# Optimization experiments

Measured on AMD Instinct MI355X. Metric: run time of the kernel, lower is better.

## Reference

```python
import jax, jax.numpy as jnp
import numpy as np

B, C_IN, C_OUT, N, K = 4, 64, 128, 81920, 10


def setup_inputs() -> dict:
    key = jax.random.key(0)
    k1, k2, k3, k4 = jax.random.split(key, 4)
    x = jax.random.normal(k1, (B, C_IN, N), dtype=jnp.float32)
    indices = jax.random.randint(k2, (N, K), 0, N, dtype=jnp.int64)
    # Conv2d(in, out, kernel=(1,K)) weight [C_out, C_in, 1, K] -> store as [C_out, C_in, K]
    fan_in = C_IN * K
    bound = 1.0 / np.sqrt(fan_in)
    W = jax.random.uniform(k3, (C_OUT, C_IN, K), jnp.float32, -bound, bound)
    b = jax.random.uniform(k4, (C_OUT,), jnp.float32, -bound, bound)
    return {"input": x, "indices": indices, "W": W, "b": b}


def reference(input, indices, W, b):
    # gather neighbor pixels: [B, C_in, N, K]
    col = input[:, :, indices]
    # 1xK conv == contraction over (C_in, K): [B, C_out, N]
    out = jnp.einsum('bcnk,ock->bon', col, W) + b[None, :, None]
    return out
```

## Files before the change

### kernel.cpp

```cpp
#include <hip/hip_runtime.h>
#include <hip/hip_bf16.h>
#include <stdint.h>

#define NPTS 81920
#define CIN  64
#define COUT 128
#define BATCH 4
#define KNB  10
#define CK   640
#define NT   64

typedef __attribute__((ext_vector_type(8))) short bf16x8;
typedef __attribute__((ext_vector_type(4))) float f32x4;

static __device__ __forceinline__ unsigned short f2bf(float f) {
    unsigned int u = __float_as_uint(f);
    u += 0x7fffu + ((u >> 16) & 1u);
    return (unsigned short)(u >> 16);
}

static __device__ __forceinline__ void gload16(const void* g, void* l) {
    __builtin_amdgcn_global_load_lds(
        (const __attribute__((address_space(1))) unsigned int*)g,
        (__attribute__((address_space(3))) unsigned int*)l, 16, 0, 0);
}

__global__ __launch_bounds__(256) void k_transpose(const float* __restrict__ x,
                                                   unsigned short* __restrict__ xT) {
    const int m = blockIdx.x * 256 + threadIdx.x;
    const int b = blockIdx.y;
    const float* xb = x + (size_t)b * CIN * NPTS + m;

    unsigned int v[CIN / 2];
    #pragma unroll
    for (int i = 0; i < CIN / 2; ++i) {
        float f0 = xb[(size_t)(2 * i) * NPTS];
        float f1 = xb[(size_t)(2 * i + 1) * NPTS];
        v[i] = (unsigned int)f2bf(f0) | ((unsigned int)f2bf(f1) << 16);
    }
    uint4* dst = (uint4*)(xT + ((size_t)m * BATCH + b) * CIN);
    #pragma unroll
    for (int i = 0; i < 8; ++i) {
        uint4 w; w.x = v[4*i]; w.y = v[4*i+1]; w.z = v[4*i+2]; w.w = v[4*i+3];
        dst[i] = w;
    }
}

__global__ __launch_bounds__(256) void k_wconv(const float* __restrict__ W,
                                               unsigned short* __restrict__ Wb) {
    const int e = blockIdx.x * 256 + threadIdx.x;
    const int j = e & 7;
    const int l = (e >> 3) & 63;
    const int f = (e >> 9) & 7;
    const int s = e >> 12;
    const int o = 16 * f + (l & 15);
    const int ck = s * 32 + 8 * (l >> 4) + j;
    const int k = ck >> 6;
    const int c = ck & 63;
    Wb[e] = f2bf(W[(o * CIN + c) * KNB + k]);
}

__global__ __launch_bounds__(512, 4) void k_main(const unsigned short* __restrict__ xT,
                                                 const unsigned short* __restrict__ Wb,
                                                 const float* __restrict__ bias,
                                                 const int* __restrict__ idx,
                                                 float* __restrict__ out) {
    __shared__ char smem[2][NT][256];

    const int t    = threadIdx.x;
    const int lane = t & 63;
    const int wv   = t >> 6;
    const int ln   = lane & 15;
    const int lg   = lane >> 4;
    const int bz   = blockIdx.y;
    const int nb   = blockIdx.x * NT;

    const char* xbase = (const char*)xT + bz * 256;
    const bf16x8* wbase = (const bf16x8*)Wb;

    f32x4 acc[4][2];
    #pragma unroll
    for (int j = 0; j < 4; ++j) {
        acc[j][0] = (f32x4){0.f, 0.f, 0.f, 0.f};
        acc[j][1] = (f32x4){0.f, 0.f, 0.f, 0.f};
    }

    #define STAGE(k)                                                            \
        {                                                                       \
            _Pragma("unroll")                                                   \
            for (int i = 0; i < 2; ++i) {                                       \
                const int row   = (wv << 3) + (i << 2) + (lane >> 4);           \
                const int nglob = nb + row;                                     \
                const int r     = idx[nglob * KNB + (k)];                       \
                const char* src = xbase + (size_t)r * 512 +                     \
                                  (((lane & 15) * 16) ^ ((row & 7) << 4));      \
                gload16(src, &smem[(k) & 1][(wv << 3) + (i << 2)][0]);          \
            }                                                                   \
        }

    STAGE(0);
    bf16x8 a0 = wbase[(0 * 8 + wv) * 64 + lane];
    bf16x8 a1 = wbase[(1 * 8 + wv) * 64 + lane];
    __syncthreads();

    #pragma unroll
    for (int k = 0; k < KNB; ++k) {
        if (k + 1 < KNB) STAGE(k + 1);
        bf16x8 a0n = a0, a1n = a1;
        if (k + 1 < KNB) {
            a0n = wbase[((2 * k + 2) * 8 + wv) * 64 + lane];
            a1n = wbase[((2 * k + 3) * 8 + wv) * 64 + lane];
        }
        #pragma unroll
        for (int h = 0; h < 2; ++h) {
            const bf16x8 a = h ? a1 : a0;
            #pragma unroll
            for (int j = 0; j < 4; ++j) {
                const int row = j * 16 + ln;
                const int sw  = (row & 7) << 4;
                #pragma unroll
                for (int bb = 0; bb < 2; ++bb) {
                    const int byte = bb * 128 + ((h * 64 + lg * 16) ^ sw);
                    const bf16x8 bf = *(const bf16x8*)&smem[k & 1][row][byte];
                    acc[j][bb] = __builtin_amdgcn_mfma_f32_16x16x32_bf16(
                        a, bf, acc[j][bb], 0, 0, 0);
                }
            }
        }
        __syncthreads();
        a0 = a0n; a1 = a1n;
    }
    #undef STAGE

    #pragma unroll
    for (int j = 0; j < 4; ++j) {
        const int n = nb + j * 16 + ln;
        #pragma unroll
        for (int bb = 0; bb < 2; ++bb) {
            const int b = bz * 2 + bb;
            #pragma unroll
            for (int r = 0; r < 4; ++r) {
                const int o = 16 * wv + 4 * lg + r;
                out[(size_t)(b * COUT + o) * NPTS + n] = acc[j][bb][r] + bias[o];
            }
        }
    }
}

extern "C" void kernel_launch(void* const* d_in, const int* in_sizes, int n_in,
                              void* d_out, int out_size, void* d_ws, size_t ws_size,
                              hipStream_t stream) {
    const float* x    = (const float*)d_in[0];
    const int*   idx  = (const int*)d_in[1];
    const float* W    = (const float*)d_in[2];
    const float* bias = (const float*)d_in[3];
    float* out = (float*)d_out;

    unsigned short* xT = (unsigned short*)d_ws;
    unsigned short* Wb = (unsigned short*)((char*)d_ws + (size_t)BATCH * NPTS * CIN * 2);

    k_transpose<<<dim3(NPTS / 256, BATCH), 256, 0, stream>>>(x, xT);
    k_wconv<<<dim3((COUT * CK) / 256), 256, 0, stream>>>(W, Wb);
    k_main<<<dim3(NPTS / NT, 2), 512, 0, stream>>>(xT, Wb, bias, idx, out);
}
```

Baseline: 133.1 us.

## Switch main kernel to 32x32x16 MFMA with 128-point tiles and chunked LDS layout

The main kernel now uses 32x32x16 bf16 MFMA instead of 16x16x32, and each block covers 128 points instead of 64. The 8 waves are split into 4 output-channel groups by 2 point halves. The weight prepack and the LDS staging layout are rebuilt to match: gathered rows go into a chunk-major layout without XOR swizzling. The aim is fewer MFMA issues per FLOP, better reuse of each weight fragment, and half as many blocks. The trade-offs are higher register pressure from 16-wide accumulators, 64KB of LDS per block which limits occupancy, and possible LDS bank conflicts now that the swizzle is gone.

```diff
diff --git a/kernel.cpp b/kernel.cpp
--- a/kernel.cpp
+++ b/kernel.cpp
@@ -7,11 +7,10 @@
 #define COUT 128
 #define BATCH 4
 #define KNB  10
-#define CK   640
-#define NT   64
+#define NT   128
 
-typedef __attribute__((ext_vector_type(8))) short bf16x8;
-typedef __attribute__((ext_vector_type(4))) float f32x4;
+typedef __attribute__((ext_vector_type(8)))  short bf16x8;
+typedef __attribute__((ext_vector_type(16))) float f32x16;
 
 static __device__ __forceinline__ unsigned short f2bf(float f) {
     unsigned int u = __float_as_uint(f);
@@ -48,16 +47,16 @@
 
 __global__ __launch_bounds__(256) void k_wconv(const float* __restrict__ W,
                                                unsigned short* __restrict__ Wb) {
-    const int e = blockIdx.x * 256 + threadIdx.x;
-    const int j = e & 7;
-    const int l = (e >> 3) & 63;
-    const int f = (e >> 9) & 7;
-    const int s = e >> 12;
-    const int o = 16 * f + (l & 15);
-    const int ck = s * 32 + 8 * (l >> 4) + j;
-    const int k = ck >> 6;
-    const int c = ck & 63;
-    Wb[e] = f2bf(W[(o * CIN + c) * KNB + k]);
+    const int e  = blockIdx.x * 256 + threadIdx.x;
+    const int j  = e & 7;
+    const int l  = (e >> 3) & 63;
+    const int f  = (e >> 9) & 3;
+    const int sg = e >> 11;
+    const int o  = 32 * f + (l & 31);
+    const int ck = sg * 16 + 8 * (l >> 5) + j;
+    const int kn = ck >> 6;
+    const int c  = ck & 63;
+    Wb[e] = f2bf(W[(o * CIN + c) * KNB + kn]);
 }
 
 __global__ __launch_bounds__(512, 4) void k_main(const unsigned short* __restrict__ xT,
@@ -65,83 +64,95 @@
                                                  const float* __restrict__ bias,
                                                  const int* __restrict__ idx,
                                                  float* __restrict__ out) {
-    __shared__ char smem[2][NT][256];
+    __shared__ char smem[2][32 * 1024];
 
     const int t    = threadIdx.x;
     const int lane = t & 63;
     const int wv   = t >> 6;
-    const int ln   = lane & 15;
-    const int lg   = lane >> 4;
+    const int ow   = wv & 3;
+    const int nh   = wv >> 2;
+    const int hw   = lane >> 5;
+    const int l31  = lane & 31;
     const int bz   = blockIdx.y;
     const int nb   = blockIdx.x * NT;
 
-    const char* xbase = (const char*)xT + bz * 256;
+    const char* xb = (const char*)xT + bz * 256;
     const bf16x8* wbase = (const bf16x8*)Wb;
 
-    f32x4 acc[4][2];
+    f32x16 acc[2][2];
     #pragma unroll
-    for (int j = 0; j < 4; ++j) {
-        acc[j][0] = (f32x4){0.f, 0.f, 0.f, 0.f};
-        acc[j][1] = (f32x4){0.f, 0.f, 0.f, 0.f};
-    }
+    for (int nf = 0; nf < 2; ++nf)
+        #pragma unroll
+        for (int bb = 0; bb < 2; ++bb)
+            #pragma unroll
+            for (int r = 0; r < 16; ++r) acc[nf][bb][r] = 0.f;
 
-    #define STAGE(k)                                                            \
+    #define STAGE(kk, buf)                                                      \
         {                                                                       \
+            const int r0 = idx[(nb + lane) * KNB + (kk)];                       \
+            const int r1 = idx[(nb + 64 + lane) * KNB + (kk)];                  \
             _Pragma("unroll")                                                   \
-            for (int i = 0; i < 2; ++i) {                                       \
-                const int row   = (wv << 3) + (i << 2) + (lane >> 4);           \
-                const int nglob = nb + row;                                     \
-                const int r     = idx[nglob * KNB + (k)];                       \
-                const char* src = xbase + (size_t)r * 512 +                     \
-                                  (((lane & 15) * 16) ^ ((row & 7) << 4));      \
-                gload16(src, &smem[(k) & 1][(wv << 3) + (i << 2)][0]);          \
+            for (int i = 0; i < 4; ++i) {                                       \
+                const int chunk = (wv << 1) + (i >> 1);                         \
+                const int rh    = i & 1;                                        \
+                const int r     = rh ? r1 : r0;                                 \
+                const char* src = xb + (size_t)r * 512 +                        \
+                                  ((chunk >> 3) << 7) + ((chunk & 7) << 4);     \
+                gload16(src, &smem[buf][(chunk << 11) + (rh << 10)]);           \
             }                                                                   \
         }
 
-    STAGE(0);
-    bf16x8 a0 = wbase[(0 * 8 + wv) * 64 + lane];
-    bf16x8 a1 = wbase[(1 * 8 + wv) * 64 + lane];
+    bf16x8 a[4], an[4];
+    STAGE(0, 0);
+    #pragma unroll
+    for (int ks = 0; ks < 4; ++ks)
+        a[ks] = wbase[((0 * 4 + ks) * 4 + ow) * 64 + lane];
     __syncthreads();
 
     #pragma unroll
     for (int k = 0; k < KNB; ++k) {
-        if (k + 1 < KNB) STAGE(k + 1);
-        bf16x8 a0n = a0, a1n = a1;
         if (k + 1 < KNB) {
-            a0n = wbase[((2 * k + 2) * 8 + wv) * 64 + lane];
-            a1n = wbase[((2 * k + 3) * 8 + wv) * 64 + lane];
+            STAGE(k + 1, (k + 1) & 1);
+            #pragma unroll
+            for (int ks = 0; ks < 4; ++ks)
+                an[ks] = wbase[(((k + 1) * 4 + ks) * 4 + ow) * 64 + lane];
         }
+        const char* sb = smem[k & 1];
         #pragma unroll
-        for (int h = 0; h < 2; ++h) {
-            const bf16x8 a = h ? a1 : a0;
+        for (int ks = 0; ks < 4; ++ks) {
             #pragma unroll
-            for (int j = 0; j < 4; ++j) {
-                const int row = j * 16 + ln;
-                const int sw  = (row & 7) << 4;
+            for (int nf = 0; nf < 2; ++nf) {
+                const int row = nh * 64 + nf * 32 + l31;
                 #pragma unroll
                 for (int bb = 0; bb < 2; ++bb) {
-                    const int byte = bb * 128 + ((h * 64 + lg * 16) ^ sw);
-                    const bf16x8 bf = *(const bf16x8*)&smem[k & 1][row][byte];
-                    acc[j][bb] = __builtin_amdgcn_mfma_f32_16x16x32_bf16(
-                        a, bf, acc[j][bb], 0, 0, 0);
+                    const int chunk = bb * 8 + ks * 2 + hw;
+                    const bf16x8 bf = *(const bf16x8*)(sb + chunk * 2048 + row * 16);
+                    acc[nf][bb] = __builtin_amdgcn_mfma_f32_32x32x16_bf16(
+                        a[ks], bf, acc[nf][bb], 0, 0, 0);
                 }
             }
         }
         __syncthreads();
-        a0 = a0n; a1 = a1n;
+        #pragma unroll
+        for (int ks = 0; ks < 4; ++ks) a[ks] = an[ks];
     }
     #undef STAGE
 
+    float bv[16];
     #pragma unroll
-    for (int j = 0; j < 4; ++j) {
-        const int n = nb + j * 16 + ln;
+    for (int r = 0; r < 16; ++r)
+        bv[r] = bias[32 * ow + (r & 3) + 8 * (r >> 2) + 4 * hw];
+
+    #pragma unroll
+    for (int nf = 0; nf < 2; ++nf) {
+        const int n = nb + nh * 64 + nf * 32 + l31;
         #pragma unroll
         for (int bb = 0; bb < 2; ++bb) {
             const int b = bz * 2 + bb;
             #pragma unroll
-            for (int r = 0; r < 4; ++r) {
-                const int o = 16 * wv + 4 * lg + r;
-                out[(size_t)(b * COUT + o) * NPTS + n] = acc[j][bb][r] + bias[o];
+            for (int r = 0; r < 16; ++r) {
+                const int o = 32 * ow + (r & 3) + 8 * (r >> 2) + 4 * hw;
+                out[(size_t)(b * COUT + o) * NPTS + n] = acc[nf][bb][r] + bv[r];
             }
         }
     }
@@ -160,6 +171,6 @@
     unsigned short* Wb = (unsigned short*)((char*)d_ws + (size_t)BATCH * NPTS * CIN * 2);
 
     k_transpose<<<dim3(NPTS / 256, BATCH), 256, 0, stream>>>(x, xT);
-    k_wconv<<<dim3((COUT * CK) / 256), 256, 0, stream>>>(W, Wb);
+    k_wconv<<<dim3((COUT * KNB * CIN) / 256), 256, 0, stream>>>(W, Wb);
     k_main<<<dim3(NPTS / NT, 2), 512, 0, stream>>>(xT, Wb, bias, idx, out);
 }
```

Measured after the change: 160.8 us. 1.21x slower.
